# Optimization experiments

Measured on AMD Instinct MI355X. Metric: run time of the kernel, lower is better.

## Reference

```python
import jax, jax.numpy as jnp
import numpy as np

BATCH, SEQ, IN, HID, OUT = 4096, 512, 2, 128, 1


def setup_inputs() -> dict:
    key = jax.random.key(0)
    k_x, k_wih, k_bih, k_who, k_bho = jax.random.split(key, 5)
    s = 1.0 / np.sqrt(IN + HID)
    return {
        "x": jax.random.normal(k_x, (BATCH, SEQ, IN), dtype=jnp.float32),
        "W_ih": jax.random.normal(k_wih, (HID, IN + HID), dtype=jnp.float32) * s,
        "b_ih": jax.random.normal(k_bih, (HID,), dtype=jnp.float32) * s,
        "W_ho": jax.random.normal(k_who, (OUT, HID), dtype=jnp.float32) / np.sqrt(HID),
        "b_bho" if False else "b_ho": jax.random.normal(k_bho, (OUT,), dtype=jnp.float32) / np.sqrt(HID),
    }


def reference(x, W_ih, b_ih, W_ho, b_ho):
    # x: [B, T, I]. Elman cell: h = tanh([x_t, h] @ W_ih^T + b_ih)
    B = x.shape[0]
    h0 = jnp.zeros((B, W_ih.shape[0]), dtype=x.dtype)
    # split W_ih into input and hidden blocks (equivalent to concat+matmul)
    W_x = W_ih[:, : x.shape[-1]]   # [H, I]
    W_h = W_ih[:, x.shape[-1] :]   # [H, H]

    def step(h, x_t):
        h_new = jnp.tanh(x_t @ W_x.T + h @ W_h.T + b_ih)
        return h_new, None

    xs = jnp.swapaxes(x, 0, 1)  # [T, B, I] for scan over time
    h_final, _ = jax.lax.scan(step, h0, xs)
    return h_final @ W_ho.T + b_ho  # [B, OUT]
```

## Files before the change

### kernel.cpp

```cpp
#include <hip/hip_runtime.h>


constexpr int BATCH   = 4096;
constexpr int SEQ     = 512;
constexpr int INP     = 2;
constexpr int HID     = 128;
constexpr int BM      = 16;
constexpr int THREADS = 512;
constexpr int XCHUNK  = 128;

typedef short bf16x8 __attribute__((ext_vector_type(8)));
typedef float f32x4  __attribute__((ext_vector_type(4)));

__device__ inline unsigned short f2bf(float f) {
    unsigned u = __float_as_uint(f);
    return (unsigned short)((u + 0x7FFFu + ((u >> 16) & 1u)) >> 16);
}
__device__ inline float bf2f(unsigned short s) {
    return __uint_as_float(((unsigned)s) << 16);
}

__global__ __launch_bounds__(THREADS, 2)
void elman_mfma_kernel(const float* __restrict__ x,
                       const float* __restrict__ W_ih,
                       const float* __restrict__ b_ih,
                       const float* __restrict__ W_ho,
                       const float* __restrict__ b_ho,
                       float* __restrict__ out)
{
    __shared__ unsigned short hlds[2][2][BM][HID];
    __shared__ float xs[BM][XCHUNK][INP];
    __shared__ float red[BM][8];

    const int tid  = threadIdx.x;
    const int lane = tid & 63;
    const int w    = tid >> 6;
    const int l15  = lane & 15;
    const int g    = lane >> 4;
    const int j    = w * 16 + l15;
    const int B0   = blockIdx.x * BM;

    bf16x8 bhi[4], blo[4];
    {
        const float* Wrow = W_ih + (size_t)j * (INP + HID) + INP;
        #pragma unroll
        for (int kt = 0; kt < 4; ++kt) {
            const int k0 = kt * 32 + g * 8;
            #pragma unroll
            for (int i = 0; i < 8; ++i) {
                const float wv = Wrow[k0 + i];
                const unsigned short hi = f2bf(wv);
                const float lo = wv - bf2f(hi);
                bhi[kt][i] = (short)hi;
                blo[kt][i] = (short)f2bf(lo);
            }
        }
    }
    const float* Wrow0 = W_ih + (size_t)j * (INP + HID);
    const float wx0 = Wrow0[0];
    const float wx1 = Wrow0[1];
    const float bj  = b_ih[j];

    reinterpret_cast<float4*>(hlds)[tid] = float4{0.f, 0.f, 0.f, 0.f};

    {
        const int row = tid >> 5;
        const int o8  = (tid & 31) * 8;
        const float* src = x + (size_t)(B0 + row) * (SEQ * INP) + o8;
        float* dst = &xs[row][0][0] + o8;
        *reinterpret_cast<float4*>(dst)     = *reinterpret_cast<const float4*>(src);
        *reinterpret_cast<float4*>(dst + 4) = *reinterpret_cast<const float4*>(src + 4);
    }
    __syncthreads();

    int p = 0;
    float hv[4] = {0.f, 0.f, 0.f, 0.f};
    const int sw_r = (l15 & 7) << 4;

    #pragma unroll 1
    for (int t = 0; t < SEQ; ++t) {
        const int tt = t & (XCHUNK - 1);
        if (t && tt == 0) {
            const int row = tid >> 5;
            const int o8  = (tid & 31) * 8;
            const float* src = x + (size_t)(B0 + row) * (SEQ * INP)
                                 + (size_t)(t >> 7) * (XCHUNK * INP) + o8;
            float* dst = &xs[row][0][0] + o8;
            *reinterpret_cast<float4*>(dst)     = *reinterpret_cast<const float4*>(src);
            *reinterpret_cast<float4*>(dst + 4) = *reinterpret_cast<const float4*>(src + 4);
            __syncthreads();
        }

        const char* hp = (const char*)&hlds[p][0][0][0];
        const char* lp = (const char*)&hlds[p][1][0][0];
        bf16x8 ahi[4], alo[4];
        #pragma unroll
        for (int kt = 0; kt < 4; ++kt) {
            const int off = l15 * 256 + ((kt * 64 + g * 16) ^ sw_r);
            ahi[kt] = *reinterpret_cast<const bf16x8*>(hp + off);
            alo[kt] = *reinterpret_cast<const bf16x8*>(lp + off);
        }

        f32x4 a0 = {0.f, 0.f, 0.f, 0.f};
        f32x4 a1 = {0.f, 0.f, 0.f, 0.f};
        f32x4 a2 = {0.f, 0.f, 0.f, 0.f};
        #pragma unroll
        for (int kt = 0; kt < 4; ++kt) {
            a0 = __builtin_amdgcn_mfma_f32_16x16x32_bf16(ahi[kt], bhi[kt], a0, 0, 0, 0);
            a1 = __builtin_amdgcn_mfma_f32_16x16x32_bf16(alo[kt], bhi[kt], a1, 0, 0, 0);
            a2 = __builtin_amdgcn_mfma_f32_16x16x32_bf16(ahi[kt], blo[kt], a2, 0, 0, 0);
        }

        unsigned short* hn = &hlds[p ^ 1][0][0][0];
        unsigned short* ln = &hlds[p ^ 1][1][0][0];
        #pragma unroll
        for (int i = 0; i < 4; ++i) {
            const int rr = g * 4 + i;
            const float2 xv = *reinterpret_cast<const float2*>(&xs[rr][tt][0]);
            const float acc = (a0[i] + a1[i] + a2[i])
                            + fmaf(wx0, xv.x, fmaf(wx1, xv.y, bj));
            const float e = __expf(2.0f * acc);
            const float h = 1.0f - __fdividef(2.0f, e + 1.0f);
            hv[i] = h;
            const unsigned short hb = f2bf(h);
            const float lo = h - bf2f(hb);
            const int off = rr * 256 + ((2 * j) ^ ((rr & 7) << 4));
            *(unsigned short*)((char*)hn + off) = hb;
            *(unsigned short*)((char*)ln + off) = f2bf(lo);
        }
        __syncthreads();
        p ^= 1;
    }

    const float who = W_ho[j];
    float pr[4];
    #pragma unroll
    for (int i = 0; i < 4; ++i) {
        float v = who * hv[i];
        v += __shfl_xor(v, 1);
        v += __shfl_xor(v, 2);
        v += __shfl_xor(v, 4);
        v += __shfl_xor(v, 8);
        pr[i] = v;
    }
    if (l15 == 0) {
        #pragma unroll
        for (int i = 0; i < 4; ++i) red[g * 4 + i][w] = pr[i];
    }
    __syncthreads();
    if (tid < BM) {
        float s = b_ho[0];
        #pragma unroll
        for (int q = 0; q < 8; ++q) s += red[tid][q];
        out[B0 + tid] = s;
    }
}

extern "C" void kernel_launch(void* const* d_in, const int* in_sizes, int n_in,
                              void* d_out, int out_size, void* d_ws, size_t ws_size,
                              hipStream_t stream)
{
    (void)in_sizes; (void)n_in; (void)out_size; (void)d_ws; (void)ws_size;
    const float* x    = (const float*)d_in[0];
    const float* W_ih = (const float*)d_in[1];
    const float* b_ih = (const float*)d_in[2];
    const float* W_ho = (const float*)d_in[3];
    const float* b_ho = (const float*)d_in[4];
    float* out = (float*)d_out;

    dim3 grid(BATCH / BM);
    dim3 block(THREADS);
    elman_mfma_kernel<<<grid, block, 0, stream>>>(x, W_ih, b_ih, W_ho, b_ho, out);
}
```

Before: 374.4 us.

## Interleave hi/lo bf16 hidden state in LDS and use packed bf16 converts

Hidden state hi and lo bf16 parts are stored interleaved per element, so one 32-bit LDS write stores both. The A operand then spans a K of 256 (hi and lo interleaved) with B weights duplicated to match, and an 8-step K loop of two MFMAs each replaces the three-product split. Rounding uses the hardware v_cvt_pk_bf16_f32 instruction, and LDS offsets are precomputed outside the loop. The aim is fewer LDS stores and less ALU work per step on the recurrent critical path. The total MFMA count rises from 12 to 16 per step and the x staging buffer gets padded rows.

New measurement: 420.5 us. +12.3%, slower.

```diff
diff --git a/kernel.cpp b/kernel.cpp
--- a/kernel.cpp
+++ b/kernel.cpp
@@ -8,28 +8,28 @@
 constexpr int BM      = 16;
 constexpr int THREADS = 512;
 constexpr int XCHUNK  = 128;
+constexpr int XROW    = XCHUNK * INP + 4;
 
 typedef short bf16x8 __attribute__((ext_vector_type(8)));
 typedef float f32x4  __attribute__((ext_vector_type(4)));
+typedef unsigned int u32x4 __attribute__((ext_vector_type(4)));
 
-__device__ inline unsigned short f2bf(float f) {
-    unsigned u = __float_as_uint(f);
-    return (unsigned short)((u + 0x7FFFu + ((u >> 16) & 1u)) >> 16);
-}
-__device__ inline float bf2f(unsigned short s) {
-    return __uint_as_float(((unsigned)s) << 16);
+__device__ inline unsigned cvt_pk_bf16(float a, float b) {
+    unsigned r;
+    asm("v_cvt_pk_bf16_f32 %0, %1, %2" : "=v"(r) : "v"(a), "v"(b));
+    return r;
 }
 
 __global__ __launch_bounds__(THREADS, 2)
-void elman_mfma_kernel(const float* __restrict__ x,
-                       const float* __restrict__ W_ih,
-                       const float* __restrict__ b_ih,
-                       const float* __restrict__ W_ho,
-                       const float* __restrict__ b_ho,
-                       float* __restrict__ out)
+void elman_mfma2(const float* __restrict__ x,
+                 const float* __restrict__ W_ih,
+                 const float* __restrict__ b_ih,
+                 const float* __restrict__ W_ho,
+                 const float* __restrict__ b_ho,
+                 float* __restrict__ out)
 {
-    __shared__ unsigned short hlds[2][2][BM][HID];
-    __shared__ float xs[BM][XCHUNK][INP];
+    __shared__ unsigned short hlds[2][BM][2 * HID];
+    __shared__ float xs[BM][XROW];
     __shared__ float red[BM][8];
 
     const int tid  = threadIdx.x;
@@ -40,20 +40,24 @@
     const int j    = w * 16 + l15;
     const int B0   = blockIdx.x * BM;
 
-    bf16x8 bhi[4], blo[4];
+    bf16x8 Bhi[8], Blo[8];
     {
         const float* Wrow = W_ih + (size_t)j * (INP + HID) + INP;
         #pragma unroll
-        for (int kt = 0; kt < 4; ++kt) {
-            const int k0 = kt * 32 + g * 8;
+        for (int kt = 0; kt < 8; ++kt) {
+            const float4 wv = *reinterpret_cast<const float4*>(Wrow + kt * 16 + g * 4);
+            const float wm[4] = {wv.x, wv.y, wv.z, wv.w};
+            u32x4 hi, lo;
             #pragma unroll
-            for (int i = 0; i < 8; ++i) {
-                const float wv = Wrow[k0 + i];
-                const unsigned short hi = f2bf(wv);
-                const float lo = wv - bf2f(hi);
-                bhi[kt][i] = (short)hi;
-                blo[kt][i] = (short)f2bf(lo);
+            for (int m = 0; m < 4; ++m) {
+                const unsigned c1 = cvt_pk_bf16(wm[m], wm[m]);
+                const float whf = __uint_as_float(c1 << 16);
+                const float wl  = wm[m] - whf;
+                hi[m] = c1;
+                lo[m] = cvt_pk_bf16(wl, wl);
             }
+            Bhi[kt] = __builtin_bit_cast(bf16x8, hi);
+            Blo[kt] = __builtin_bit_cast(bf16x8, lo);
         }
     }
     const float* Wrow0 = W_ih + (size_t)j * (INP + HID);
@@ -61,72 +65,73 @@
     const float wx1 = Wrow0[1];
     const float bj  = b_ih[j];
 
+    int roff[8];
+    #pragma unroll
+    for (int kt = 0; kt < 8; ++kt)
+        roff[kt] = l15 * 512 + ((kt * 64 + g * 16) ^ ((l15 & 7) << 4));
+    int woff[4];
+    #pragma unroll
+    for (int i = 0; i < 4; ++i) {
+        const int rr = g * 4 + i;
+        woff[i] = rr * 512 + ((4 * j) ^ ((rr & 7) << 4));
+    }
+
     reinterpret_cast<float4*>(hlds)[tid] = float4{0.f, 0.f, 0.f, 0.f};
 
+    const int sr = tid >> 5;
+    const int sc = (tid & 31) * 4;
     {
-        const int row = tid >> 5;
-        const int o8  = (tid & 31) * 8;
-        const float* src = x + (size_t)(B0 + row) * (SEQ * INP) + o8;
-        float* dst = &xs[row][0][0] + o8;
-        *reinterpret_cast<float4*>(dst)     = *reinterpret_cast<const float4*>(src);
-        *reinterpret_cast<float4*>(dst + 4) = *reinterpret_cast<const float4*>(src + 4);
+        const float* src = x + (size_t)(B0 + sr) * (SEQ * INP) + sc;
+        *reinterpret_cast<float4*>(&xs[sr][sc])       = *reinterpret_cast<const float4*>(src);
+        *reinterpret_cast<float4*>(&xs[sr][sc + 128]) = *reinterpret_cast<const float4*>(src + 128);
     }
     __syncthreads();
 
+    const char* hb0 = (const char*)&hlds[0][0][0];
+    const char* hb1 = (const char*)&hlds[1][0][0];
     int p = 0;
     float hv[4] = {0.f, 0.f, 0.f, 0.f};
-    const int sw_r = (l15 & 7) << 4;
 
     #pragma unroll 1
     for (int t = 0; t < SEQ; ++t) {
         const int tt = t & (XCHUNK - 1);
         if (t && tt == 0) {
-            const int row = tid >> 5;
-            const int o8  = (tid & 31) * 8;
-            const float* src = x + (size_t)(B0 + row) * (SEQ * INP)
-                                 + (size_t)(t >> 7) * (XCHUNK * INP) + o8;
-            float* dst = &xs[row][0][0] + o8;
-            *reinterpret_cast<float4*>(dst)     = *reinterpret_cast<const float4*>(src);
-            *reinterpret_cast<float4*>(dst + 4) = *reinterpret_cast<const float4*>(src + 4);
+            const float* src = x + (size_t)(B0 + sr) * (SEQ * INP)
+                                 + (size_t)(t >> 7) * (XCHUNK * INP) + sc;
+            *reinterpret_cast<float4*>(&xs[sr][sc])       = *reinterpret_cast<const float4*>(src);
+            *reinterpret_cast<float4*>(&xs[sr][sc + 128]) = *reinterpret_cast<const float4*>(src + 128);
             __syncthreads();
         }
 
-        const char* hp = (const char*)&hlds[p][0][0][0];
-        const char* lp = (const char*)&hlds[p][1][0][0];
-        bf16x8 ahi[4], alo[4];
+        const char* hp = p ? hb1 : hb0;
+        bf16x8 A[8];
         #pragma unroll
-        for (int kt = 0; kt < 4; ++kt) {
-            const int off = l15 * 256 + ((kt * 64 + g * 16) ^ sw_r);
-            ahi[kt] = *reinterpret_cast<const bf16x8*>(hp + off);
-            alo[kt] = *reinterpret_cast<const bf16x8*>(lp + off);
-        }
+        for (int kt = 0; kt < 8; ++kt)
+            A[kt] = *reinterpret_cast<const bf16x8*>(hp + roff[kt]);
 
         f32x4 a0 = {0.f, 0.f, 0.f, 0.f};
         f32x4 a1 = {0.f, 0.f, 0.f, 0.f};
-        f32x4 a2 = {0.f, 0.f, 0.f, 0.f};
         #pragma unroll
-        for (int kt = 0; kt < 4; ++kt) {
-            a0 = __builtin_amdgcn_mfma_f32_16x16x32_bf16(ahi[kt], bhi[kt], a0, 0, 0, 0);
-            a1 = __builtin_amdgcn_mfma_f32_16x16x32_bf16(alo[kt], bhi[kt], a1, 0, 0, 0);
-            a2 = __builtin_amdgcn_mfma_f32_16x16x32_bf16(ahi[kt], blo[kt], a2, 0, 0, 0);
+        for (int kt = 0; kt < 8; ++kt) {
+            a0 = __builtin_amdgcn_mfma_f32_16x16x32_bf16(A[kt], Bhi[kt], a0, 0, 0, 0);
+            a1 = __builtin_amdgcn_mfma_f32_16x16x32_bf16(A[kt], Blo[kt], a1, 0, 0, 0);
         }
 
-        unsigned short* hn = &hlds[p ^ 1][0][0][0];
-        unsigned short* ln = &hlds[p ^ 1][1][0][0];
+        char* wp = (char*)(p ? hb0 : hb1);
         #pragma unroll
         for (int i = 0; i < 4; ++i) {
             const int rr = g * 4 + i;
-            const float2 xv = *reinterpret_cast<const float2*>(&xs[rr][tt][0]);
-            const float acc = (a0[i] + a1[i] + a2[i])
+            const float2 xv = *reinterpret_cast<const float2*>(&xs[rr][2 * tt]);
+            const float acc = (a0[i] + a1[i])
                             + fmaf(wx0, xv.x, fmaf(wx1, xv.y, bj));
-            const float e = __expf(2.0f * acc);
+            const float e = __expf(acc + acc);
             const float h = 1.0f - __fdividef(2.0f, e + 1.0f);
             hv[i] = h;
-            const unsigned short hb = f2bf(h);
-            const float lo = h - bf2f(hb);
-            const int off = rr * 256 + ((2 * j) ^ ((rr & 7) << 4));
-            *(unsigned short*)((char*)hn + off) = hb;
-            *(unsigned short*)((char*)ln + off) = f2bf(lo);
+            const unsigned c1  = cvt_pk_bf16(h, h);
+            const float    hbf = __uint_as_float(c1 << 16);
+            const float    lo  = h - hbf;
+            const unsigned c2  = cvt_pk_bf16(h, lo);
+            *reinterpret_cast<unsigned*>(wp + woff[i]) = c2;
         }
         __syncthreads();
         p ^= 1;
@@ -170,5 +175,5 @@
 
     dim3 grid(BATCH / BM);
     dim3 block(THREADS);
-    elman_mfma_kernel<<<grid, block, 0, stream>>>(x, W_ih, b_ih, W_ho, b_ho, out);
+    elman_mfma2<<<grid, block, 0, stream>>>(x, W_ih, b_ih, W_ho, b_ho, out);
 }
```
